# Performance work log

Measured on AMD Instinct MI355X. Metric: run time of the kernel, lower is better.

Reference implementation:

```python
import jax, jax.numpy as jnp
import numpy as np
from functools import partial

N_ITER = 200  # LML(n_iter=200)


def sq_dists(Xi, x):
    # Xi: [N, n], x: [B, n] -> squared euclidean dists [B, N] (torch.cdist ** 2)
    x2 = jnp.sum(x * x, axis=1, keepdims=True)          # [B, 1]
    m2 = jnp.sum(Xi * Xi, axis=1)                        # [N]
    d = x2 + m2[None, :] - 2.0 * (x @ Xi.T)
    return jnp.maximum(d, 0.0)


def _lml_solve(x, k):
    # LML projection: y = sigmoid(x + nu), nu s.t. sum(y) = k; bisection on nu.
    x_sorted = -jnp.sort(-x, axis=1)                     # descending
    lo = -x_sorted[:, k - 1] - 7.0
    hi = -x_sorted[:, k] + 7.0

    def body(i, bounds):
        lo, hi = bounds
        mid = 0.5 * (lo + hi)
        f = jnp.sum(jax.nn.sigmoid(x + mid[:, None]), axis=1) - k
        lo = jnp.where(f < 0, mid, lo)
        hi = jnp.where(f < 0, hi, mid)
        return lo, hi

    lo, hi = jax.lax.fori_loop(0, N_ITER, body, (lo, hi))
    nu = 0.5 * (lo + hi)
    return jax.nn.sigmoid(x + nu[:, None])


@partial(jax.custom_vjp, nondiff_argnums=(1,))
def lml(x, k):
    return _lml_solve(x, k)


def _lml_fwd(x, k):
    y = _lml_solve(x, k)
    return y, y


def _lml_bwd(k, y, g):
    # implicit grad: dy = s*(dx - dnu), dnu = sum(s*dx)/sum(s), s = y(1-y)
    s = y * (1.0 - y)
    dnu = jnp.sum(s * g, axis=1, keepdims=True) / jnp.sum(s, axis=1, keepdims=True)
    return (s * (g - dnu),)


lml.defvjp(_lml_fwd, _lml_bwd)


def k_softmax(beta, x, k):
    # x: [B, N] (= -dists) -> [B, N, k]
    cols = [jax.nn.softmax(beta * x, axis=1)]
    last = cols[0]
    for i in range(1, k):
        new = lml(beta * x, i + 1)
        cols.append(new - last)
        last = new
    return jnp.stack(cols, axis=2)


def hopfield(Xi, x, beta):
    return jax.nn.softmax(-beta * sq_dists(Xi, x), axis=1) @ Xi


def k_hopfield_batch(Xi, x, k, beta, hopfield_steps):
    dists = sq_dists(Xi, x)                              # [B, N]
    ksm = k_softmax(beta, -dists, k)                     # [B, N, k]
    result = jnp.einsum('nd,bnk->bdk', Xi, ksm)          # Xi.T @ ksm -> [B, n, k]
    for _ in range(hopfield_steps):
        result = jnp.stack(
            [hopfield(Xi, result[:, :, j], beta) for j in range(k)], axis=2)
    return result


def setup_inputs() -> dict:
    key = jax.random.key(0)
    kx, km = jax.random.split(key)
    return {
        'x': jax.random.normal(kx, (2048, 512), dtype=jnp.float32),
        'memories': jax.random.normal(km, (8192, 512), dtype=jnp.float32),
        'k': 5,
        'beta': 1,
        'hopfield_steps': 2,
    }


def reference(x, memories, k, beta, hopfield_steps):
    return k_hopfield_batch(memories, x, k, beta, hopfield_steps)
```

## Files before the change

### kernel.cpp

```cpp
#include <hip/hip_runtime.h>
#include <hip/hip_bf16.h>


constexpr int   Bq    = 2048;
constexpr int   Nm    = 8192;
constexpr int   Dd    = 512;
constexpr int   KK    = 5;
constexpr float BETA  = 1.0f;
constexpr int   STEPS = 2;
constexpr int   KS    = 8;
constexpr size_t PL   = (size_t)Bq * Dd;

#define DEV static __device__ __forceinline__

DEV float b2f(ushort u) { unsigned v = ((unsigned)u) << 16; float f; __builtin_memcpy(&f, &v, 4); return f; }
DEV ushort f2b(float f) { __hip_bfloat16 h = __float2bfloat16(f); ushort u; __builtin_memcpy(&u, &h, 2); return u; }
DEV float ldin(const void* p, int isf, size_t idx) {
    return isf ? ((const float*)p)[idx] : b2f(((const ushort*)p)[idx]);
}

__global__ __launch_bounds__(256) void detect_k(const ushort* __restrict__ xin,
                                                int* __restrict__ flag) {
    __shared__ int sb;
    if (threadIdx.x == 0) sb = 0;
    __syncthreads();
    int bad = 0;
    for (int i = threadIdx.x; i < 1024; i += 256) {
        float v = b2f(xin[i]);
        if (!(fabsf(v) < 64.0f)) bad = 1;
    }
    if (bad) atomicOr(&sb, 1);
    __syncthreads();
    if (threadIdx.x == 0) flag[0] = sb;
}

__global__ __launch_bounds__(256) void norms_k(const void* __restrict__ xin,
                                               const void* __restrict__ memin,
                                               const int* __restrict__ flag,
                                               float* __restrict__ x2,
                                               float* __restrict__ m2) {
    int row = blockIdx.x;
    int isf = flag[0];
    const void* src; size_t base; float* dst;
    if (row < Nm) { src = memin; base = (size_t)row * Dd; dst = m2 + row; }
    else          { src = xin; base = (size_t)(row - Nm) * Dd; dst = x2 + (row - Nm); }
    int tid = threadIdx.x, lane = tid & 63, wave = tid >> 6;
    float s = 0.f;
    for (int i = tid; i < Dd; i += 256) { float v = ldin(src, isf, base + i); s += v * v; }
    for (int off = 32; off; off >>= 1) s += __shfl_down(s, off, 64);
    __shared__ float ws[4];
    if (lane == 0) ws[wave] = s;
    __syncthreads();
    if (tid == 0) dst[0] = ws[0] + ws[1] + ws[2] + ws[3];
}

__global__ __launch_bounds__(256) void distF2_k(const void* __restrict__ A,
                                                const int* __restrict__ flag, int aForceF,
                                                const void* __restrict__ memin,
                                                float* __restrict__ S,
                                                const float* __restrict__ a2,
                                                const float* __restrict__ m2,
                                                int ab0, float negBeta) {
    __shared__ float As[16][68];
    __shared__ float Bs[16][68];
    const int tid = threadIdx.x, tx = tid & 15, ty = tid >> 4;
    const int m0 = blockIdx.y * 64, n0 = blockIdx.x * 64;
    const int isfA = aForceF ? 1 : flag[0];
    const int isfB = flag[0];

    float acc[4][4];
#pragma unroll
    for (int i = 0; i < 4; ++i)
#pragma unroll
        for (int j = 0; j < 4; ++j) acc[i][j] = 0.f;

    for (int d0 = 0; d0 < Dd; d0 += 16) {
#pragma unroll
        for (int c = tid; c < 1024; c += 256) {
            int r = c >> 4, k = c & 15;
            As[k][r] = ldin(A, isfA, (size_t)(ab0 + m0 + r) * Dd + d0 + k);
            Bs[k][r] = ldin(memin, isfB, (size_t)(n0 + r) * Dd + d0 + k);
        }
        __syncthreads();
#pragma unroll
        for (int k = 0; k < 16; ++k) {
            float4 av = *(const float4*)&As[k][ty * 4];
            float4 bv = *(const float4*)&Bs[k][tx * 4];
            float a[4] = {av.x, av.y, av.z, av.w};
            float b[4] = {bv.x, bv.y, bv.z, bv.w};
#pragma unroll
            for (int i = 0; i < 4; ++i)
#pragma unroll
                for (int j = 0; j < 4; ++j) acc[i][j] = fmaf(a[i], b[j], acc[i][j]);
        }
        __syncthreads();
    }
#pragma unroll
    for (int i = 0; i < 4; ++i) {
        int m = m0 + ty * 4 + i;
        float4 o;
        float* po = (float*)&o;
#pragma unroll
        for (int j = 0; j < 4; ++j) {
            float d = a2[m] + m2[n0 + tx * 4 + j] - 2.0f * acc[i][j];
            po[j] = negBeta * fmaxf(d, 0.0f);
        }
        *(float4*)&S[(size_t)m * Nm + n0 + tx * 4] = o;
    }
}

template <int TRF>
__global__ __launch_bounds__(256) void wgemmG_k(const float* __restrict__ Sx,
                                                const void* __restrict__ memin,
                                                const int* __restrict__ flag,
                                                const float* __restrict__ rowpar,
                                                float* __restrict__ part, int planeSz) {
    __shared__ float Ws[16][68];
    __shared__ float Bs[16][68];
    const int tid = threadIdx.x, tx = tid & 15, ty = tid >> 4;
    const int d0 = blockIdx.x * 64, b0 = blockIdx.y * 64;
    const int kz = blockIdx.z * (Nm / KS);
    const int isf = flag[0];

    float acc[4][4];
#pragma unroll
    for (int i = 0; i < 4; ++i)
#pragma unroll
        for (int j = 0; j < 4; ++j) acc[i][j] = 0.f;

    for (int nc = kz; nc < kz + Nm / KS; nc += 16) {
#pragma unroll
        for (int c = tid; c < 1024; c += 256) {
            int r = c >> 4, k = c & 15;
            float s = Sx[(size_t)(b0 + r) * Nm + nc + k];
            float p0 = rowpar[(b0 + r) * 2 + 0];
            float w;
            if constexpr (TRF == 1) w = expf(s - p0) * rowpar[(b0 + r) * 2 + 1];
            else                    w = 1.0f / (1.0f + expf(-(s + p0)));
            Ws[k][r] = w;
            int kk = c >> 6, dd = c & 63;
            Bs[kk][dd] = ldin(memin, isf, (size_t)(nc + kk) * Dd + d0 + dd);
        }
        __syncthreads();
#pragma unroll
        for (int k = 0; k < 16; ++k) {
            float4 av = *(const float4*)&Ws[k][ty * 4];
            float4 bv = *(const float4*)&Bs[k][tx * 4];
            float a[4] = {av.x, av.y, av.z, av.w};
            float b[4] = {bv.x, bv.y, bv.z, bv.w};
#pragma unroll
            for (int i = 0; i < 4; ++i)
#pragma unroll
                for (int j = 0; j < 4; ++j) acc[i][j] = fmaf(a[i], b[j], acc[i][j]);
        }
        __syncthreads();
    }
    float* pz = part + (size_t)blockIdx.z * planeSz;
#pragma unroll
    for (int i = 0; i < 4; ++i) {
        float4 o = {acc[i][0], acc[i][1], acc[i][2], acc[i][3]};
        *(float4*)&pz[(size_t)(b0 + ty * 4 + i) * Dd + d0 + tx * 4] = o;
    }
}

__global__ __launch_bounds__(256) void reduceN_k(const float* __restrict__ part,
                                                 float* __restrict__ Rj,
                                                 float* __restrict__ r2w, int doNorm,
                                                 int planeSz) {
    int row = blockIdx.x, tid = threadIdx.x, lane = tid & 63, wave = tid >> 6;
    float sq = 0.f;
    for (int e = tid; e < Dd; e += 256) {
        float s = 0.f;
#pragma unroll
        for (int z = 0; z < KS; ++z) s += part[(size_t)z * planeSz + (size_t)row * Dd + e];
        Rj[(size_t)row * Dd + e] = s;
        sq += s * s;
    }
    if (doNorm) {
        for (int off = 32; off; off >>= 1) sq += __shfl_down(sq, off, 64);
        __shared__ float ws[4];
        if (lane == 0) ws[wave] = sq;
        __syncthreads();
        if (tid == 0) r2w[row] = ws[0] + ws[1] + ws[2] + ws[3];
    }
}

__global__ __launch_bounds__(256) void rowstats_k(const float* __restrict__ S,
                                                  float* __restrict__ stats) {
    int b = blockIdx.x, tid = threadIdx.x, lane = tid & 63, wave = tid >> 6;
    __shared__ float cbuf[1024];
    __shared__ int   ccnt;
    __shared__ float tops[256 * 6];
    __shared__ float stop[6];
    __shared__ float wred[16];
    __shared__ float bcast[5];
    const float* srow = S + (size_t)b * Nm;

    float tt[6];
#pragma unroll
    for (int q = 0; q < 6; ++q) tt[q] = -3.4e38f;
    for (int i = tid; i < Nm; i += 256) {
        float v = srow[i];
        if (v > tt[5]) {
            tt[5] = v;
#pragma unroll
            for (int q = 5; q > 0; --q)
                if (tt[q] > tt[q - 1]) { float tm = tt[q]; tt[q] = tt[q - 1]; tt[q - 1] = tm; }
        }
    }
#pragma unroll
    for (int q = 0; q < 6; ++q) tops[tid * 6 + q] = tt[q];
    if (tid == 0) ccnt = 0;
    __syncthreads();
    if (tid == 0) {
        float mt[6];
#pragma unroll
        for (int q = 0; q < 6; ++q) mt[q] = -3.4e38f;
        for (int i = 0; i < 256 * 6; ++i) {
            float v = tops[i];
            if (v > mt[5]) {
                mt[5] = v;
#pragma unroll
                for (int q = 5; q > 0; --q)
                    if (mt[q] > mt[q - 1]) { float tm = mt[q]; mt[q] = mt[q - 1]; mt[q - 1] = tm; }
            }
        }
#pragma unroll
        for (int q = 0; q < 6; ++q) stop[q] = mt[q];
    }
    __syncthreads();

    float smax = stop[0];
    float cutoff = stop[5] - 40.0f;
    float p = 0.f;
    for (int i = tid; i < Nm; i += 256) {
        float v = srow[i];
        p += expf(v - smax);
        if (v >= cutoff) {
            int idx = atomicAdd(&ccnt, 1);
            if (idx < 1024) cbuf[idx] = v;
        }
    }
    for (int off = 32; off; off >>= 1) p += __shfl_down(p, off, 64);
    if (lane == 0) wred[wave] = p;
    __syncthreads();
    if (tid == 0) bcast[4] = wred[0] + wred[1] + wred[2] + wred[3];
    __syncthreads();
    float denom = bcast[4];
    int cnt = min(ccnt, 1024);

    float lo[4], hi[4];
#pragma unroll
    for (int q = 0; q < 4; ++q) { lo[q] = -stop[q + 1] - 7.0f; hi[q] = -stop[q + 2] + 7.0f; }
    for (int it = 0; it < 48; ++it) {
        float mid[4], pp[4] = {0.f, 0.f, 0.f, 0.f};
#pragma unroll
        for (int q = 0; q < 4; ++q) mid[q] = 0.5f * (lo[q] + hi[q]);
        for (int i = tid; i < cnt; i += 256) {
            float v = cbuf[i];
#pragma unroll
            for (int q = 0; q < 4; ++q) pp[q] += 1.0f / (1.0f + expf(-(v + mid[q])));
        }
#pragma unroll
        for (int q = 0; q < 4; ++q) {
            float s = pp[q];
            for (int off = 32; off; off >>= 1) s += __shfl_down(s, off, 64);
            if (lane == 0) wred[wave * 4 + q] = s;
        }
        __syncthreads();
        if (tid == 0)
#pragma unroll
            for (int q = 0; q < 4; ++q) bcast[q] = wred[q] + wred[4 + q] + wred[8 + q] + wred[12 + q];
        __syncthreads();
#pragma unroll
        for (int q = 0; q < 4; ++q) {
            float f = bcast[q] - (float)(q + 2);
            if (f < 0.f) lo[q] = mid[q]; else hi[q] = mid[q];
        }
        __syncthreads();
    }
    if (tid == 0) {
        stats[b * 6 + 0] = smax;
        stats[b * 6 + 1] = denom;
#pragma unroll
        for (int q = 0; q < 4; ++q) stats[b * 6 + 2 + q] = 0.5f * (lo[q] + hi[q]);
    }
}

__global__ __launch_bounds__(256) void rowpar_stage1_k(const float* __restrict__ stats,
                                                       float* __restrict__ rowpar, int jj) {
    int b = blockIdx.x * 256 + threadIdx.x;
    if (b >= Bq) return;
    if (jj == 0) {
        rowpar[b * 2 + 0] = stats[b * 6 + 0];
        rowpar[b * 2 + 1] = 1.0f / stats[b * 6 + 1];
    } else {
        rowpar[b * 2 + 0] = stats[b * 6 + 1 + jj];
        rowpar[b * 2 + 1] = 0.0f;
    }
}

__global__ __launch_bounds__(256) void rowmax_denom_k(const float* __restrict__ S,
                                                      float* __restrict__ rowpar) {
    int b = blockIdx.x, tid = threadIdx.x, lane = tid & 63, wave = tid >> 6;
    __shared__ float wred[4];
    __shared__ float bc[1];
    const float* srow = S + (size_t)b * Nm;
    float mx = -3.4e38f;
    for (int i = tid; i < Nm; i += 256) mx = fmaxf(mx, srow[i]);
    for (int off = 32; off; off >>= 1) mx = fmaxf(mx, __shfl_down(mx, off, 64));
    if (lane == 0) wred[wave] = mx;
    __syncthreads();
    if (tid == 0) bc[0] = fmaxf(fmaxf(wred[0], wred[1]), fmaxf(wred[2], wred[3]));
    __syncthreads();
    mx = bc[0];
    float p = 0.f;
    for (int i = tid; i < Nm; i += 256) p += expf(srow[i] - mx);
    for (int off = 32; off; off >>= 1) p += __shfl_down(p, off, 64);
    __syncthreads();
    if (lane == 0) wred[wave] = p;
    __syncthreads();
    if (tid == 0) {
        rowpar[b * 2 + 0] = mx;
        rowpar[b * 2 + 1] = 1.0f / (wred[0] + wred[1] + wred[2] + wred[3]);
    }
}

__global__ __launch_bounds__(256) void combine_k(float* __restrict__ R,
                                                 float* __restrict__ r2all) {
    int row = blockIdx.x, tid = threadIdx.x, lane = tid & 63, wave = tid >> 6;
    float sq[5] = {0.f, 0.f, 0.f, 0.f, 0.f};
    for (int e = tid; e < Dd; e += 256) {
        size_t idx = (size_t)row * Dd + e;
        float r0 = R[idx], r1 = R[PL + idx], r2v = R[2 * PL + idx],
              r3 = R[3 * PL + idx], r4 = R[4 * PL + idx];
        float o1 = r1 - r0, o2 = r2v - r1, o3 = r3 - r2v, o4 = r4 - r3;
        R[PL + idx] = o1; R[2 * PL + idx] = o2; R[3 * PL + idx] = o3; R[4 * PL + idx] = o4;
        sq[0] += r0 * r0; sq[1] += o1 * o1; sq[2] += o2 * o2; sq[3] += o3 * o3; sq[4] += o4 * o4;
    }
    __shared__ float ws[5][4];
#pragma unroll
    for (int j = 0; j < 5; ++j) {
        float s = sq[j];
        for (int off = 32; off; off >>= 1) s += __shfl_down(s, off, 64);
        if (lane == 0) ws[j][wave] = s;
    }
    __syncthreads();
    if (tid < 5) r2all[tid * Bq + row] = ws[tid][0] + ws[tid][1] + ws[tid][2] + ws[tid][3];
}

__global__ __launch_bounds__(256) void final_k(const float* __restrict__ R,
                                               void* __restrict__ out,
                                               const int* __restrict__ flag) {
    size_t idx = (size_t)blockIdx.x * 256 + threadIdx.x;
    bool isf = flag[0] != 0;
#pragma unroll
    for (int j = 0; j < KK; ++j) {
        float v = R[(size_t)j * PL + idx];
        if (isf) ((float*)out)[idx * KK + j] = v;
        else     ((ushort*)out)[idx * KK + j] = f2b(v);
    }
}

extern "C" void kernel_launch(void* const* d_in, const int* in_sizes, int n_in,
                              void* d_out, int out_size, void* d_ws, size_t ws_size,
                              hipStream_t stream) {
    const void* xin   = d_in[0];
    const void* memin = d_in[1];

    const size_t MiB = 1048576ull, KiB = 1024ull;
    char* ws = (char*)d_ws;
    float* R     = (float*)(ws + 0);
    float* m2    = (float*)(ws + 20 * MiB);
    float* x2    = (float*)(ws + 20 * MiB + 32 * KiB);
    float* stats = (float*)(ws + 20 * MiB + 48 * KiB);
    float* rpar  = (float*)(ws + 20 * MiB + 96 * KiB);
    int*   flag  = (int*)  (ws + 20 * MiB + 112 * KiB);
    float* r2all = (float*)(ws + 20 * MiB + 128 * KiB);
    float* S     = (float*)(ws + 20 * MiB + 256 * KiB);

    float* part = (float*)d_out;

    int Bc = 128;
    const int cand[4] = {1024, 512, 256, 128};
    for (int i = 0; i < 4; ++i)
        if (20 * MiB + 256 * KiB + (size_t)cand[i] * Nm * 4 <= ws_size) { Bc = cand[i]; break; }
    const int nChunk = Bq / Bc;
    const int planeSz = Bc * Dd;

    detect_k<<<1, 256, 0, stream>>>((const ushort*)xin, flag);
    norms_k<<<Nm + Bq, 256, 0, stream>>>(xin, memin, flag, x2, m2);

    for (int c = 0; c < nChunk; ++c) {
        int b0 = c * Bc;
        distF2_k<<<dim3(Nm / 64, Bc / 64), 256, 0, stream>>>(
            xin, flag, 0, memin, S, x2 + b0, m2, b0, -BETA);
        rowstats_k<<<Bc, 256, 0, stream>>>(S, stats + (size_t)b0 * 6);
        for (int jj = 0; jj < KK; ++jj) {
            float* Rj = R + (size_t)jj * PL + (size_t)b0 * Dd;
            rowpar_stage1_k<<<Bq / 256, 256, 0, stream>>>(stats, rpar, jj);
            if (jj == 0)
                wgemmG_k<1><<<dim3(Dd / 64, Bc / 64, KS), 256, 0, stream>>>(
                    S, memin, flag, rpar + (size_t)b0 * 2, part, planeSz);
            else
                wgemmG_k<2><<<dim3(Dd / 64, Bc / 64, KS), 256, 0, stream>>>(
                    S, memin, flag, rpar + (size_t)b0 * 2, part, planeSz);
            reduceN_k<<<Bc, 256, 0, stream>>>(part, Rj, nullptr, 0, planeSz);
        }
    }
    combine_k<<<Bq, 256, 0, stream>>>(R, r2all);

    for (int st = 0; st < STEPS; ++st) {
        for (int jj = 0; jj < KK; ++jj) {
            float* Rj = R + (size_t)jj * PL;
            float* r2j = r2all + (size_t)jj * Bq;
            for (int c = 0; c < nChunk; ++c) {
                int b0 = c * Bc;
                distF2_k<<<dim3(Nm / 64, Bc / 64), 256, 0, stream>>>(
                    Rj, flag, 1, memin, S, r2j + b0, m2, b0, -BETA);
                rowmax_denom_k<<<Bc, 256, 0, stream>>>(S, rpar + (size_t)b0 * 2);
                wgemmG_k<1><<<dim3(Dd / 64, Bc / 64, KS), 256, 0, stream>>>(
                    S, memin, flag, rpar + (size_t)b0 * 2, part, planeSz);
                reduceN_k<<<Bc, 256, 0, stream>>>(
                    part, Rj + (size_t)b0 * Dd, r2j + b0, 1, planeSz);
            }
        }
    }
    final_k<<<(int)(PL / 256), 256, 0, stream>>>(R, d_out, flag);
}
```

Baseline: 10.11 ms.

## Replace FP32 SIMT GEMMs with split-bf16 MFMA kernels using 128x128 tiles

Swaps the scalar-FMA distance GEMM and weighted GEMM for MFMA kernels. Each fp32 operand is split into bf16 high and low parts, and three bf16 MFMAs per product approximate fp32 accuracy. Tiles grow to 128x128 with swizzled LDS layouts, and the chunk-size picker now also checks that the output buffer can hold the partial planes. The aim is to move the dominant GEMM work onto matrix cores, at the cost of some precision risk, extra conversion work during staging, and uncoalesced scalar epilogue stores.

After: 15.16 ms. +50.0%, slower.

```diff
diff --git a/kernel.cpp b/kernel.cpp
--- a/kernel.cpp
+++ b/kernel.cpp
@@ -12,6 +12,10 @@
 constexpr size_t PL   = (size_t)Bq * Dd;
 
 #define DEV static __device__ __forceinline__
+
+typedef __attribute__((ext_vector_type(8))) short           short8v;
+typedef __attribute__((ext_vector_type(8))) unsigned short  u16x8;
+typedef __attribute__((ext_vector_type(4))) float           f32x4;
 
 DEV float b2f(ushort u) { unsigned v = ((unsigned)u) << 16; float f; __builtin_memcpy(&f, &v, 4); return f; }
 DEV ushort f2b(float f) { __hip_bfloat16 h = __float2bfloat16(f); ushort u; __builtin_memcpy(&u, &h, 2); return u; }
@@ -54,113 +58,197 @@
     if (tid == 0) dst[0] = ws[0] + ws[1] + ws[2] + ws[3];
 }
 
-__global__ __launch_bounds__(256) void distF2_k(const void* __restrict__ A,
+
+DEV void writeHL(const float* v, int r, int h, ushort* H, ushort* L) {
+    u16x8 hv[2], lv[2];
+#pragma unroll
+    for (int c = 0; c < 2; ++c)
+#pragma unroll
+        for (int j = 0; j < 8; ++j) {
+            float x  = v[c * 8 + j];
+            ushort hu = f2b(x);
+            float  hf = b2f(hu);
+            hv[c][j] = hu;
+            lv[c][j] = f2b(x - hf);
+        }
+    const int s = (r >> 1) & 3;
+#pragma unroll
+    for (int c = 0; c < 2; ++c) {
+        const int pc = (2 * h + c) ^ s;
+        *(u16x8*)&H[r * 32 + pc * 8] = hv[c];
+        *(u16x8*)&L[r * 32 + pc * 8] = lv[c];
+    }
+}
+
+DEV void stageAB(const void* src, int isf, int row0, int k0,
+                 ushort* H, ushort* L, int tid) {
+    const int r = tid >> 1, h = tid & 1;
+    const size_t base = (size_t)(row0 + r) * Dd + k0 + h * 16;
+    float v[16];
+    if (isf) {
+        const float4* p = (const float4*)((const float*)src + base);
+#pragma unroll
+        for (int i = 0; i < 4; ++i) {
+            float4 t = p[i];
+            v[i * 4 + 0] = t.x; v[i * 4 + 1] = t.y; v[i * 4 + 2] = t.z; v[i * 4 + 3] = t.w;
+        }
+    } else {
+        const u16x8* p = (const u16x8*)((const ushort*)src + base);
+        u16x8 t0 = p[0], t1 = p[1];
+#pragma unroll
+        for (int j = 0; j < 8; ++j) { v[j] = b2f(t0[j]); v[8 + j] = b2f(t1[j]); }
+    }
+    writeHL(v, r, h, H, L);
+}
+
+template <int TRF>
+DEV void stageW(const float* Sx, const float* rowpar, int b0, int nc,
+                ushort* H, ushort* L, int tid) {
+    const int r = tid >> 1, h = tid & 1;
+    const float* sp = &Sx[(size_t)(b0 + r) * Nm + nc + h * 16];
+    const float p0 = rowpar[(b0 + r) * 2 + 0];
+    const float p1 = rowpar[(b0 + r) * 2 + 1];
+    float v[16];
+#pragma unroll
+    for (int i = 0; i < 4; ++i) {
+        float4 t = ((const float4*)sp)[i];
+        float s4[4] = {t.x, t.y, t.z, t.w};
+#pragma unroll
+        for (int j = 0; j < 4; ++j) {
+            float s = s4[j];
+            v[i * 4 + j] = (TRF == 1) ? expf(s - p0) * p1
+                                      : 1.0f / (1.0f + expf(-(s + p0)));
+        }
+    }
+    writeHL(v, r, h, H, L);
+}
+
+DEV void stageBT(const void* memin, int isf, int d0, int nc,
+                 ushort* H, ushort* L, int tid) {
+    const int d = tid & 127, h = tid >> 7;
+    float v[16];
+#pragma unroll
+    for (int nn = 0; nn < 16; ++nn)
+        v[nn] = ldin(memin, isf, (size_t)(nc + h * 16 + nn) * Dd + d0 + d);
+    writeHL(v, d, h, H, L);
+}
+
+DEV short8v rdfrag(const ushort* T, int row, int kc) {
+    const int pc = kc ^ ((row >> 1) & 3);
+    return *(const short8v*)&T[row * 32 + pc * 8];
+}
+
+DEV void mfma_block(const ushort* AHt, const ushort* ALt,
+                    const ushort* BHt, const ushort* BLt,
+                    int lane, int wm, int wn, f32x4 (&acc)[4][4]) {
+    const int rl = lane & 15, kc = lane >> 4;
+    short8v ah[4], al[4];
+#pragma unroll
+    for (int fm = 0; fm < 4; ++fm) {
+        const int rowa = wm * 64 + fm * 16 + rl;
+        ah[fm] = rdfrag(AHt, rowa, kc);
+        al[fm] = rdfrag(ALt, rowa, kc);
+    }
+#pragma unroll
+    for (int fn = 0; fn < 4; ++fn) {
+        const int rowb = wn * 64 + fn * 16 + rl;
+        short8v bh = rdfrag(BHt, rowb, kc);
+        short8v bl = rdfrag(BLt, rowb, kc);
+#pragma unroll
+        for (int fm = 0; fm < 4; ++fm) {
+            acc[fm][fn] = __builtin_amdgcn_mfma_f32_16x16x32_bf16(ah[fm], bh, acc[fm][fn], 0, 0, 0);
+            acc[fm][fn] = __builtin_amdgcn_mfma_f32_16x16x32_bf16(al[fm], bh, acc[fm][fn], 0, 0, 0);
+            acc[fm][fn] = __builtin_amdgcn_mfma_f32_16x16x32_bf16(ah[fm], bl, acc[fm][fn], 0, 0, 0);
+        }
+    }
+}
+
+__global__ __launch_bounds__(256) void distMF_k(const void* __restrict__ A,
                                                 const int* __restrict__ flag, int aForceF,
                                                 const void* __restrict__ memin,
                                                 float* __restrict__ S,
                                                 const float* __restrict__ a2,
                                                 const float* __restrict__ m2,
                                                 int ab0, float negBeta) {
-    __shared__ float As[16][68];
-    __shared__ float Bs[16][68];
-    const int tid = threadIdx.x, tx = tid & 15, ty = tid >> 4;
-    const int m0 = blockIdx.y * 64, n0 = blockIdx.x * 64;
+    __shared__ ushort AH[4096], AL[4096], BH[4096], BL[4096];
+    const int tid = threadIdx.x, lane = tid & 63, wid = tid >> 6;
+    const int wm = wid >> 1, wn = wid & 1;
+    const int m0 = blockIdx.y * 128, n0 = blockIdx.x * 128;
     const int isfA = aForceF ? 1 : flag[0];
     const int isfB = flag[0];
 
-    float acc[4][4];
+    f32x4 acc[4][4];
+    const f32x4 z = {0.f, 0.f, 0.f, 0.f};
 #pragma unroll
     for (int i = 0; i < 4; ++i)
 #pragma unroll
-        for (int j = 0; j < 4; ++j) acc[i][j] = 0.f;
-
-    for (int d0 = 0; d0 < Dd; d0 += 16) {
-#pragma unroll
-        for (int c = tid; c < 1024; c += 256) {
-            int r = c >> 4, k = c & 15;
-            As[k][r] = ldin(A, isfA, (size_t)(ab0 + m0 + r) * Dd + d0 + k);
-            Bs[k][r] = ldin(memin, isfB, (size_t)(n0 + r) * Dd + d0 + k);
-        }
-        __syncthreads();
-#pragma unroll
-        for (int k = 0; k < 16; ++k) {
-            float4 av = *(const float4*)&As[k][ty * 4];
-            float4 bv = *(const float4*)&Bs[k][tx * 4];
-            float a[4] = {av.x, av.y, av.z, av.w};
-            float b[4] = {bv.x, bv.y, bv.z, bv.w};
-#pragma unroll
-            for (int i = 0; i < 4; ++i)
-#pragma unroll
-                for (int j = 0; j < 4; ++j) acc[i][j] = fmaf(a[i], b[j], acc[i][j]);
-        }
-        __syncthreads();
-    }
-#pragma unroll
-    for (int i = 0; i < 4; ++i) {
-        int m = m0 + ty * 4 + i;
-        float4 o;
-        float* po = (float*)&o;
-#pragma unroll
-        for (int j = 0; j < 4; ++j) {
-            float d = a2[m] + m2[n0 + tx * 4 + j] - 2.0f * acc[i][j];
-            po[j] = negBeta * fmaxf(d, 0.0f);
-        }
-        *(float4*)&S[(size_t)m * Nm + n0 + tx * 4] = o;
-    }
+        for (int j = 0; j < 4; ++j) acc[i][j] = z;
+
+    for (int k0 = 0; k0 < Dd; k0 += 32) {
+        stageAB(A, isfA, ab0 + m0, k0, AH, AL, tid);
+        stageAB(memin, isfB, n0, k0, BH, BL, tid);
+        __syncthreads();
+        mfma_block(AH, AL, BH, BL, lane, wm, wn, acc);
+        __syncthreads();
+    }
+
+    const int col = lane & 15, r0 = (lane >> 4) * 4;
+#pragma unroll
+    for (int fm = 0; fm < 4; ++fm)
+#pragma unroll
+        for (int fn = 0; fn < 4; ++fn) {
+            const int n = n0 + wn * 64 + fn * 16 + col;
+            const float mm2 = m2[n];
+#pragma unroll
+            for (int q = 0; q < 4; ++q) {
+                const int m = m0 + wm * 64 + fm * 16 + r0 + q;
+                const float d = a2[m] + mm2 - 2.0f * acc[fm][fn][q];
+                S[(size_t)m * Nm + n] = negBeta * fmaxf(d, 0.0f);
+            }
+        }
 }
 
 template <int TRF>
-__global__ __launch_bounds__(256) void wgemmG_k(const float* __restrict__ Sx,
-                                                const void* __restrict__ memin,
-                                                const int* __restrict__ flag,
-                                                const float* __restrict__ rowpar,
-                                                float* __restrict__ part, int planeSz) {
-    __shared__ float Ws[16][68];
-    __shared__ float Bs[16][68];
-    const int tid = threadIdx.x, tx = tid & 15, ty = tid >> 4;
-    const int d0 = blockIdx.x * 64, b0 = blockIdx.y * 64;
+__global__ __launch_bounds__(256) void wgemmMF_k(const float* __restrict__ Sx,
+                                                 const void* __restrict__ memin,
+                                                 const int* __restrict__ flag,
+                                                 const float* __restrict__ rowpar,
+                                                 float* __restrict__ part, int planeSz) {
+    __shared__ ushort WH[4096], WL[4096], BH[4096], BL[4096];
+    const int tid = threadIdx.x, lane = tid & 63, wid = tid >> 6;
+    const int wm = wid >> 1, wn = wid & 1;
+    const int d0 = blockIdx.x * 128, b0 = blockIdx.y * 128;
     const int kz = blockIdx.z * (Nm / KS);
     const int isf = flag[0];
 
-    float acc[4][4];
+    f32x4 acc[4][4];
+    const f32x4 z = {0.f, 0.f, 0.f, 0.f};
 #pragma unroll
     for (int i = 0; i < 4; ++i)
 #pragma unroll
-        for (int j = 0; j < 4; ++j) acc[i][j] = 0.f;
-
-    for (int nc = kz; nc < kz + Nm / KS; nc += 16) {
-#pragma unroll
-        for (int c = tid; c < 1024; c += 256) {
-            int r = c >> 4, k = c & 15;
-            float s = Sx[(size_t)(b0 + r) * Nm + nc + k];
-            float p0 = rowpar[(b0 + r) * 2 + 0];
-            float w;
-            if constexpr (TRF == 1) w = expf(s - p0) * rowpar[(b0 + r) * 2 + 1];
-            else                    w = 1.0f / (1.0f + expf(-(s + p0)));
-            Ws[k][r] = w;
-            int kk = c >> 6, dd = c & 63;
-            Bs[kk][dd] = ldin(memin, isf, (size_t)(nc + kk) * Dd + d0 + dd);
-        }
-        __syncthreads();
-#pragma unroll
-        for (int k = 0; k < 16; ++k) {
-            float4 av = *(const float4*)&Ws[k][ty * 4];
-            float4 bv = *(const float4*)&Bs[k][tx * 4];
-            float a[4] = {av.x, av.y, av.z, av.w};
-            float b[4] = {bv.x, bv.y, bv.z, bv.w};
-#pragma unroll
-            for (int i = 0; i < 4; ++i)
-#pragma unroll
-                for (int j = 0; j < 4; ++j) acc[i][j] = fmaf(a[i], b[j], acc[i][j]);
-        }
-        __syncthreads();
-    }
+        for (int j = 0; j < 4; ++j) acc[i][j] = z;
+
+    for (int nc = kz; nc < kz + Nm / KS; nc += 32) {
+        stageW<TRF>(Sx, rowpar, b0, nc, WH, WL, tid);
+        stageBT(memin, isf, d0, nc, BH, BL, tid);
+        __syncthreads();
+        mfma_block(WH, WL, BH, BL, lane, wm, wn, acc);
+        __syncthreads();
+    }
+
     float* pz = part + (size_t)blockIdx.z * planeSz;
-#pragma unroll
-    for (int i = 0; i < 4; ++i) {
-        float4 o = {acc[i][0], acc[i][1], acc[i][2], acc[i][3]};
-        *(float4*)&pz[(size_t)(b0 + ty * 4 + i) * Dd + d0 + tx * 4] = o;
-    }
+    const int col = lane & 15, r0 = (lane >> 4) * 4;
+#pragma unroll
+    for (int fm = 0; fm < 4; ++fm)
+#pragma unroll
+        for (int fn = 0; fn < 4; ++fn) {
+            const int dc = d0 + wn * 64 + fn * 16 + col;
+#pragma unroll
+            for (int q = 0; q < 4; ++q) {
+                const int br = b0 + wm * 64 + fm * 16 + r0 + q;
+                pz[(size_t)br * Dd + dc] = acc[fm][fn][q];
+            }
+        }
 }
 
 __global__ __launch_bounds__(256) void reduceN_k(const float* __restrict__ part,
@@ -383,8 +471,11 @@
 
     int Bc = 128;
     const int cand[4] = {1024, 512, 256, 128};
-    for (int i = 0; i < 4; ++i)
-        if (20 * MiB + 256 * KiB + (size_t)cand[i] * Nm * 4 <= ws_size) { Bc = cand[i]; break; }
+    for (int i = 0; i < 4; ++i) {
+        size_t needWS  = 20 * MiB + 256 * KiB + (size_t)cand[i] * Nm * 4;
+        size_t needOut = (size_t)KS * cand[i] * Dd * 4;
+        if (needWS <= ws_size && needOut <= (size_t)out_size) { Bc = cand[i]; break; }
+    }
     const int nChunk = Bq / Bc;
     const int planeSz = Bc * Dd;
 
@@ -393,17 +484,17 @@
 
     for (int c = 0; c < nChunk; ++c) {
         int b0 = c * Bc;
-        distF2_k<<<dim3(Nm / 64, Bc / 64), 256, 0, stream>>>(
+        distMF_k<<<dim3(Nm / 128, Bc / 128), 256, 0, stream>>>(
             xin, flag, 0, memin, S, x2 + b0, m2, b0, -BETA);
         rowstats_k<<<Bc, 256, 0, stream>>>(S, stats + (size_t)b0 * 6);
         for (int jj = 0; jj < KK; ++jj) {
             float* Rj = R + (size_t)jj * PL + (size_t)b0 * Dd;
             rowpar_stage1_k<<<Bq / 256, 256, 0, stream>>>(stats, rpar, jj);
             if (jj == 0)
-                wgemmG_k<1><<<dim3(Dd / 64, Bc / 64, KS), 256, 0, stream>>>(
+                wgemmMF_k<1><<<dim3(Dd / 128, Bc / 128, KS), 256, 0, stream>>>(
                     S, memin, flag, rpar + (size_t)b0 * 2, part, planeSz);
             else
-                wgemmG_k<2><<<dim3(Dd / 64, Bc / 64, KS), 256, 0, stream>>>(
+                wgemmMF_k<2><<<dim3(Dd / 128, Bc / 128, KS), 256, 0, stream>>>(
                     S, memin, flag, rpar + (size_t)b0 * 2, part, planeSz);
             reduceN_k<<<Bc, 256, 0, stream>>>(part, Rj, nullptr, 0, planeSz);
         }
@@ -416,10 +507,10 @@
             float* r2j = r2all + (size_t)jj * Bq;
             for (int c = 0; c < nChunk; ++c) {
                 int b0 = c * Bc;
-                distF2_k<<<dim3(Nm / 64, Bc / 64), 256, 0, stream>>>(
+                distMF_k<<<dim3(Nm / 128, Bc / 128), 256, 0, stream>>>(
                     Rj, flag, 1, memin, S, r2j + b0, m2, b0, -BETA);
                 rowmax_denom_k<<<Bc, 256, 0, stream>>>(S, rpar + (size_t)b0 * 2);
-                wgemmG_k<1><<<dim3(Dd / 64, Bc / 64, KS), 256, 0, stream>>>(
+                wgemmMF_k<1><<<dim3(Dd / 128, Bc / 128, KS), 256, 0, stream>>>(
                     S, memin, flag, rpar + (size_t)b0 * 2, part, planeSz);
                 reduceN_k<<<Bc, 256, 0, stream>>>(
                     part, Rj + (size_t)b0 * Dd, r2j + b0, 1, planeSz);
```
